# Performance work log

Hardware: AMD Instinct MI355X
Metric: run time of the kernel (lower is better)

The kernel has to match this reference:

```python
import jax, jax.numpy as jnp
import numpy as np
import math

D_MODEL = 1024
NUM_HEADS = 16
D_K = D_MODEL // NUM_HEADS
MAX_SEQ_LEN = 2048
THETA = 10000.0
BATCH = 2
SEQ = 2048


def _rope_tables():
    inv_freq = THETA ** (-jnp.arange(0, D_K, 2, dtype=jnp.float32) / D_K)  # [d_k/2]
    pos = jnp.arange(MAX_SEQ_LEN, dtype=jnp.float32)                      # [max_seq]
    ang = pos[:, None] * inv_freq[None, :]                                # [max_seq, d_k/2]
    return jnp.cos(ang), jnp.sin(ang)


def _apply_rope(x, token_positions, cos_tab, sin_tab):
    # x: [b, h, s, d_k]; token_positions: [b, s]
    cos = cos_tab[token_positions][:, None, :, :]  # [b,1,s,d_k/2]
    sin = sin_tab[token_positions][:, None, :, :]
    xp = x.reshape(*x.shape[:-1], D_K // 2, 2)     # interleaved pairs
    xe, xo = xp[..., 0], xp[..., 1]
    oe = xe * cos - xo * sin
    oo = xe * sin + xo * cos
    return jnp.stack((oe, oo), axis=-1).reshape(x.shape)


def setup_inputs() -> dict:
    key = jax.random.key(0)
    ks = jax.random.split(key, 5)
    std = math.sqrt(2.0 / (D_MODEL + D_MODEL))
    x = jax.random.normal(ks[0], (BATCH, SEQ, D_MODEL), dtype=jnp.float32)
    wq = jax.random.normal(ks[1], (D_MODEL, D_MODEL), dtype=jnp.float32) * std
    wk = jax.random.normal(ks[2], (D_MODEL, D_MODEL), dtype=jnp.float32) * std
    wv = jax.random.normal(ks[3], (D_MODEL, D_MODEL), dtype=jnp.float32) * std
    wo = jax.random.normal(ks[4], (D_MODEL, D_MODEL), dtype=jnp.float32) * std
    token_positions = jnp.broadcast_to(jnp.arange(SEQ, dtype=jnp.int32), (BATCH, SEQ))
    return {"x": x, "wq": wq, "wk": wk, "wv": wv, "wo": wo,
            "token_positions": token_positions}


def reference(x, wq, wk, wv, wo, token_positions):
    b, s, _ = x.shape
    cos_tab, sin_tab = _rope_tables()

    def proj_heads(w):
        y = jnp.einsum('oi,bsi->bso', w, x)  # Linear: w[d_out,d_in]
        return y.reshape(b, s, NUM_HEADS, D_K).transpose(0, 2, 1, 3)  # [b,h,s,d_k]

    q = proj_heads(wq)
    k = proj_heads(wk)
    v = proj_heads(wv)
    q = _apply_rope(q, token_positions, cos_tab, sin_tab)
    k = _apply_rope(k, token_positions, cos_tab, sin_tab)

    scores = jnp.einsum('bhqd,bhkd->bhqk', q, k) / math.sqrt(D_K)
    causal = jnp.tril(jnp.ones((s, s), dtype=bool))
    scores = jnp.where(causal, scores, -jnp.inf)
    attn = jax.nn.softmax(scores, axis=-1)
    out = jnp.einsum('bhqk,bhkd->bhqd', attn, v)
    out = out.transpose(0, 2, 1, 3).reshape(b, s, D_MODEL)
    return jnp.einsum('oi,bsi->bso', wo, out)
```

## Files before the change

kernel.cpp:

```cpp
#include <hip/hip_runtime.h>
#include <cstdint>
#include <cstddef>

#define NH 16
#define DK 64
#define DM 1024
#define SEQL 2048
#define NB 2
#define NR (NB * SEQL)

typedef short bf16x8 __attribute__((ext_vector_type(8)));
typedef float f32x4 __attribute__((ext_vector_type(4)));

static __device__ __forceinline__ float bf2f(short u) {
  union { unsigned int i; float f; } x;
  x.i = ((unsigned int)(unsigned short)u) << 16;
  return x.f;
}
static __device__ __forceinline__ short f2bf(float f) {
  union { unsigned int i; float f; } x;
  x.f = f;
  unsigned int r = x.i + 0x7fffu + ((x.i >> 16) & 1u);
  return (short)(r >> 16);
}
static __device__ __forceinline__ unsigned pk2(float a, float b) {
  return ((unsigned)(unsigned short)f2bf(b) << 16) | (unsigned)(unsigned short)f2bf(a);
}

static __device__ __forceinline__ void store_out(float* p, float v) { *p = v; }
static __device__ __forceinline__ void store_out(short* p, float v) { *p = f2bf(v); }

static __device__ __forceinline__ void gload16(const short* g, short* l) {
  __builtin_amdgcn_global_load_lds((const __attribute__((address_space(1))) void*)g,
                                   (__attribute__((address_space(3))) void*)l, 16, 0, 0);
}

__global__ void cvt_all(const float* __restrict__ x, const float* __restrict__ w0,
                        const float* __restrict__ w1, const float* __restrict__ w2,
                        const float* __restrict__ w3, short* __restrict__ xb,
                        short* __restrict__ o0, short* __restrict__ o1,
                        short* __restrict__ o2, short* __restrict__ o3) {
  int y = blockIdx.y;
  const float* in;
  short* out;
  if (y < 4) { in = x + (size_t)y * DM * DM; out = xb + (size_t)y * DM * DM; }
  else if (y == 4) { in = w0; out = o0; }
  else if (y == 5) { in = w1; out = o1; }
  else if (y == 6) { in = w2; out = o2; }
  else { in = w3; out = o3; }
  int i = (blockIdx.x * blockDim.x + threadIdx.x) * 4;
  float4 v = *reinterpret_cast<const float4*>(in + i);
  short4 o;
  o.x = f2bf(v.x); o.y = f2bf(v.y); o.z = f2bf(v.z); o.w = f2bf(v.w);
  *reinterpret_cast<short4*>(out + i) = o;
}

__global__ void rope_table_kernel(float2* __restrict__ tab) {
  int idx = blockIdx.x * blockDim.x + threadIdx.x;
  int pos = idx >> 5, j = idx & 31;
  float freq = powf(10000.0f, -(float)j / 32.0f);
  float ang = (float)pos * freq;
  tab[idx] = make_float2(cosf(ang), sinf(ang));
}

__global__ void rope_apply_kernel(short* __restrict__ Qb, short* __restrict__ Kb,
                                  const int* __restrict__ pos, const float2* __restrict__ tab) {
  short* buf = blockIdx.y ? Kb : Qb;
  const float scale = blockIdx.y ? 1.0f : 0.1803368801f;
  int gid = blockIdx.x * blockDim.x + threadIdx.x;
  int elem = gid * 8;
  int row = elem >> 10, off = elem & 1023;
  int j0 = (off & 63) >> 1;
  short* ptr = buf + (size_t)row * DM + off;
  bf16x8 v = *reinterpret_cast<bf16x8*>(ptr);
  const float2* tp = &tab[pos[row] * 32 + j0];
  bf16x8 o;
#pragma unroll
  for (int q = 0; q < 4; ++q) {
    float2 cs = tp[q];
    float xe = bf2f(v[2 * q]), xo = bf2f(v[2 * q + 1]);
    o[2 * q] = f2bf((xe * cs.x - xo * cs.y) * scale);
    o[2 * q + 1] = f2bf((xe * cs.y + xo * cs.x) * scale);
  }
  *reinterpret_cast<bf16x8*>(ptr) = o;
}

__global__ __launch_bounds__(256) void vt_transpose_kernel(const short* __restrict__ V,
                                                           short* __restrict__ Vt) {
  __shared__ short tile[64][64];
  const int t = threadIdx.x;
  const int bh = blockIdx.y, b = bh >> 4, h = bh & 15;
  const int st = blockIdx.x * 64;
#pragma unroll
  for (int p = 0; p < 2; ++p) {
    int c = p * 256 + t;
    int srow = c >> 3, ch = c & 7;
    int chs = ch ^ ((srow >> 3) & 7);
    *reinterpret_cast<bf16x8*>(&tile[srow][chs * 8]) =
        *reinterpret_cast<const bf16x8*>(&V[(size_t)(b * SEQL + st + srow) * DM + h * 64 + ch * 8]);
  }
  __syncthreads();
#pragma unroll
  for (int p = 0; p < 2; ++p) {
    int c = p * 256 + t;
    int drow = c >> 3, soff = (c & 7) * 8;
    short o[8];
#pragma unroll
    for (int e = 0; e < 8; ++e) {
      int srow = soff + e;
      int col = (((drow >> 3) ^ ((srow >> 3) & 7)) << 3) + (drow & 7);
      o[e] = tile[srow][col];
    }
    *reinterpret_cast<bf16x8*>(&Vt[(size_t)(bh * DK + drow) * SEQL + st + soff]) =
        *reinterpret_cast<bf16x8*>(o);
  }
}

template <typename OutT>
static __device__ __forceinline__ void gemm_body(const short* __restrict__ A,
                                                 const short* __restrict__ B,
                                                 OutT* __restrict__ C,
                                                 int m0, int n0, int N, int K) {
  __shared__ short As[128][32];
  __shared__ short Bs[128][32];
  const int t = threadIdx.x;
  const int wid = t >> 6, lane = t & 63;
  const int wr = wid >> 1, wc = wid & 1;
  const int lrow = lane & 15, lk = lane >> 4;

  f32x4 acc[4][4];
#pragma unroll
  for (int i = 0; i < 4; ++i)
#pragma unroll
    for (int j = 0; j < 4; ++j) acc[i][j] = (f32x4){0.f, 0.f, 0.f, 0.f};

  for (int k0 = 0; k0 < K; k0 += 32) {
    __syncthreads();
#pragma unroll
    for (int p = 0; p < 2; ++p) {
      int c = p * 256 + t;
      int row = c >> 2, kc = (c & 3) * 8;
      gload16(&A[(size_t)(m0 + row) * K + k0 + kc], &As[0][0] + (size_t)(p * 256 + wid * 64) * 8);
      gload16(&B[(size_t)(n0 + row) * K + k0 + kc], &Bs[0][0] + (size_t)(p * 256 + wid * 64) * 8);
    }
    __syncthreads();
    bf16x8 af[4], bfr[4];
#pragma unroll
    for (int i = 0; i < 4; ++i) {
      af[i] = *reinterpret_cast<const bf16x8*>(&As[wr * 64 + i * 16 + lrow][lk * 8]);
      bfr[i] = *reinterpret_cast<const bf16x8*>(&Bs[wc * 64 + i * 16 + lrow][lk * 8]);
    }
    __builtin_amdgcn_s_setprio(1);
#pragma unroll
    for (int i = 0; i < 4; ++i)
#pragma unroll
      for (int j = 0; j < 4; ++j)
        acc[i][j] = __builtin_amdgcn_mfma_f32_16x16x32_bf16(af[i], bfr[j], acc[i][j], 0, 0, 0);
    __builtin_amdgcn_s_setprio(0);
  }
#pragma unroll
  for (int i = 0; i < 4; ++i)
#pragma unroll
    for (int j = 0; j < 4; ++j) {
      int row = m0 + wr * 64 + i * 16 + lk * 4;
      int col = n0 + wc * 64 + j * 16 + lrow;
#pragma unroll
      for (int r = 0; r < 4; ++r) store_out(&C[(size_t)(row + r) * N + col], acc[i][j][r]);
    }
}

__global__ __launch_bounds__(256) void qkv_gemm_kernel(
    const short* __restrict__ X, const short* __restrict__ Wq, const short* __restrict__ Wk,
    const short* __restrict__ Wv, short* __restrict__ Q, short* __restrict__ K,
    short* __restrict__ V) {
  int nb = blockIdx.x;
  const short* B = (nb < 8) ? Wq : (nb < 16) ? Wk : Wv;
  short* C = (nb < 8) ? Q : (nb < 16) ? K : V;
  gemm_body<short>(X, B, C, blockIdx.y * 128, (nb & 7) * 128, DM, DM);
}

__global__ __launch_bounds__(256) void out_gemm_kernel(const short* __restrict__ A,
                                                       const short* __restrict__ W,
                                                       float* __restrict__ C) {
  gemm_body<float>(A, W, C, blockIdx.y * 128, blockIdx.x * 128, DM, DM);
}

__global__ __launch_bounds__(256) void attn_kernel(const short* __restrict__ Q,
                                                   const short* __restrict__ K,
                                                   const short* __restrict__ Vt,
                                                   short* __restrict__ O) {
  __shared__ short Ks[2][64][72];
  __shared__ short Vs[2][64][72];
  __shared__ short Ps[4][16][72];
  const int t = threadIdx.x;
  const int wid = t >> 6, lane = t & 63;
  const int lrow = lane & 15, lk = lane >> 4;
  const int lin = blockIdx.x + 16 * blockIdx.y;
  const int xcd = lin & 7, idx = lin >> 3;
  const int bh = xcd * 4 + (idx >> 4);
  const int bx = idx & 15;
  const int b = bh >> 4, h = bh & 15;
  const size_t base = (size_t)b * SEQL * DM + (size_t)h * DK;
  const size_t vbase = (size_t)bh * DK * SEQL;
  const int c0 = t, c1 = 256 + t;
  const int kr0 = c0 >> 3, ko0 = (c0 & 7) * 8;
  const int kr1 = c1 >> 3, ko1 = (c1 & 7) * 8;
  const float THR = 11.5416f;

#pragma unroll
  for (int pi = 0; pi < 2; ++pi) {
    const int qt = pi ? (31 - bx) : bx;
    const int qmin = qt * 64 + wid * 16;

    bf16x8 aq[2];
#pragma unroll
    for (int c = 0; c < 2; ++c)
      aq[c] = *reinterpret_cast<const bf16x8*>(
          &Q[base + (size_t)(qmin + lrow) * DM + c * 32 + lk * 8]);

    f32x4 oacc[4];
#pragma unroll
    for (int g = 0; g < 4; ++g) oacc[g] = (f32x4){0.f, 0.f, 0.f, 0.f};
    float mrow = -1e30f, lsum = 0.f;

    __syncthreads();
    {
      bf16x8 k0 = *reinterpret_cast<const bf16x8*>(&K[base + (size_t)kr0 * DM + ko0]);
      bf16x8 k1 = *reinterpret_cast<const bf16x8*>(&K[base + (size_t)kr1 * DM + ko1]);
      bf16x8 v0 = *reinterpret_cast<const bf16x8*>(&Vt[vbase + (size_t)kr0 * SEQL + ko0]);
      bf16x8 v1 = *reinterpret_cast<const bf16x8*>(&Vt[vbase + (size_t)kr1 * SEQL + ko1]);
      *reinterpret_cast<bf16x8*>(&Ks[0][kr0][ko0]) = k0;
      *reinterpret_cast<bf16x8*>(&Ks[0][kr1][ko1]) = k1;
      *reinterpret_cast<bf16x8*>(&Vs[0][kr0][ko0]) = v0;
      *reinterpret_cast<bf16x8*>(&Vs[0][kr1][ko1]) = v1;
    }
    int cur = 0;
    bf16x8 kreg0, kreg1, vreg0, vreg1;
    for (int kt = 0; kt <= qt; ++kt) {
      __syncthreads();
      if (kt < qt) {
        size_t ko = (size_t)(kt + 1) * 64;
        kreg0 = *reinterpret_cast<const bf16x8*>(&K[base + (ko + kr0) * DM + ko0]);
        kreg1 = *reinterpret_cast<const bf16x8*>(&K[base + (ko + kr1) * DM + ko1]);
        vreg0 = *reinterpret_cast<const bf16x8*>(&Vt[vbase + (size_t)kr0 * SEQL + ko + ko0]);
        vreg1 = *reinterpret_cast<const bf16x8*>(&Vt[vbase + (size_t)kr1 * SEQL + ko + ko1]);
      }
      const bool active = (kt * 64 <= qmin + 15);
      if (active) {
        f32x4 st[4];
        __builtin_amdgcn_s_setprio(1);
#pragma unroll
        for (int g = 0; g < 4; ++g) {
          bf16x8 kf0 = *reinterpret_cast<const bf16x8*>(&Ks[cur][g * 16 + lrow][lk * 8]);
          bf16x8 kf1 = *reinterpret_cast<const bf16x8*>(&Ks[cur][g * 16 + lrow][32 + lk * 8]);
          f32x4 z = (f32x4){0.f, 0.f, 0.f, 0.f};
          z = __builtin_amdgcn_mfma_f32_16x16x32_bf16(kf0, aq[0], z, 0, 0, 0);
          st[g] = __builtin_amdgcn_mfma_f32_16x16x32_bf16(kf1, aq[1], z, 0, 0, 0);
        }
        __builtin_amdgcn_s_setprio(0);
        const int qg = qmin + lrow;
        if (kt == qt) {
#pragma unroll
          for (int g = 0; g < 4; ++g)
#pragma unroll
            for (int r = 0; r < 4; ++r)
              if (kt * 64 + g * 16 + lk * 4 + r > qg) st[g][r] = -1e30f;
        }
        float pmax = st[0][0];
#pragma unroll
        for (int g = 0; g < 4; ++g)
#pragma unroll
          for (int r = 0; r < 4; ++r) pmax = fmaxf(pmax, st[g][r]);
        if (!__all(pmax <= mrow + THR)) {
          float mx = pmax;
          mx = fmaxf(mx, __shfl_xor(mx, 16));
          mx = fmaxf(mx, __shfl_xor(mx, 32));
          float mnew = fmaxf(mrow, mx);
          float alpha = exp2f(mrow - mnew);
          lsum *= alpha;
          float alr[4];
#pragma unroll
          for (int r = 0; r < 4; ++r) alr[r] = __shfl(alpha, lk * 4 + r);
#pragma unroll
          for (int g = 0; g < 4; ++g)
#pragma unroll
            for (int r = 0; r < 4; ++r) oacc[g][r] *= alr[r];
          mrow = mnew;
        }
        float p[4][4], psum = 0.f;
#pragma unroll
        for (int g = 0; g < 4; ++g)
#pragma unroll
          for (int r = 0; r < 4; ++r) {
            float e = exp2f(st[g][r] - mrow);
            p[g][r] = e;
            psum += e;
          }
        lsum += psum;
#pragma unroll
        for (int g = 0; g < 4; ++g) {
          uint2 wv = make_uint2(pk2(p[g][0], p[g][1]), pk2(p[g][2], p[g][3]));
          *reinterpret_cast<uint2*>(&Ps[wid][lrow][g * 16 + lk * 4]) = wv;
        }
        asm volatile("s_waitcnt lgkmcnt(0)" ::: "memory");
        __builtin_amdgcn_sched_barrier(0);
        bf16x8 pa0 = *reinterpret_cast<const bf16x8*>(&Ps[wid][lrow][lk * 8]);
        bf16x8 pa1 = *reinterpret_cast<const bf16x8*>(&Ps[wid][lrow][32 + lk * 8]);
        __builtin_amdgcn_s_setprio(1);
#pragma unroll
        for (int g = 0; g < 4; ++g) {
          bf16x8 vf0 = *reinterpret_cast<const bf16x8*>(&Vs[cur][g * 16 + lrow][lk * 8]);
          bf16x8 vf1 = *reinterpret_cast<const bf16x8*>(&Vs[cur][g * 16 + lrow][32 + lk * 8]);
          oacc[g] = __builtin_amdgcn_mfma_f32_16x16x32_bf16(pa0, vf0, oacc[g], 0, 0, 0);
          oacc[g] = __builtin_amdgcn_mfma_f32_16x16x32_bf16(pa1, vf1, oacc[g], 0, 0, 0);
        }
        __builtin_amdgcn_s_setprio(0);
      }
      if (kt < qt) {
        *reinterpret_cast<bf16x8*>(&Ks[cur ^ 1][kr0][ko0]) = kreg0;
        *reinterpret_cast<bf16x8*>(&Ks[cur ^ 1][kr1][ko1]) = kreg1;
        *reinterpret_cast<bf16x8*>(&Vs[cur ^ 1][kr0][ko0]) = vreg0;
        *reinterpret_cast<bf16x8*>(&Vs[cur ^ 1][kr1][ko1]) = vreg1;
      }
      cur ^= 1;
    }
    lsum += __shfl_xor(lsum, 16);
    lsum += __shfl_xor(lsum, 32);
    float lr[4];
#pragma unroll
    for (int r = 0; r < 4; ++r) lr[r] = 1.0f / __shfl(lsum, lk * 4 + r);
#pragma unroll
    for (int g = 0; g < 4; ++g)
#pragma unroll
      for (int r = 0; r < 4; ++r)
        O[base + (size_t)(qmin + lk * 4 + r) * DM + g * 16 + lrow] = f2bf(oacc[g][r] * lr[r]);
  }
}

extern "C" void kernel_launch(void* const* d_in, const int* in_sizes, int n_in,
                              void* d_out, int out_size, void* d_ws, size_t ws_size,
                              hipStream_t stream) {
  const float* x = (const float*)d_in[0];
  const float* wq = (const float*)d_in[1];
  const float* wk = (const float*)d_in[2];
  const float* wv = (const float*)d_in[3];
  const float* wo = (const float*)d_in[4];
  const int* tpos = (const int*)d_in[5];
  float* out = (float*)d_out;

  char* w = (char*)d_ws;
  short* xb = (short*)w;  w += (size_t)NR * DM * 2;
  short* wqb = (short*)w; w += (size_t)DM * DM * 2;
  short* wkb = (short*)w; w += (size_t)DM * DM * 2;
  short* wvb = (short*)w; w += (size_t)DM * DM * 2;
  short* wob = (short*)w; w += (size_t)DM * DM * 2;
  short* Qb = (short*)w;  w += (size_t)NR * DM * 2;
  short* Kb = (short*)w;  w += (size_t)NR * DM * 2;
  short* Vb = (short*)w;  w += (size_t)NR * DM * 2;
  short* Ob = (short*)w;  w += (size_t)NR * DM * 2;
  float2* tab = (float2*)w;
  short* Vtb = xb;

  cvt_all<<<dim3(DM * DM / 1024, 8), 256, 0, stream>>>(x, wq, wk, wv, wo, xb, wqb, wkb, wvb, wob);
  rope_table_kernel<<<2048 * 32 / 256, 256, 0, stream>>>(tab);
  qkv_gemm_kernel<<<dim3(24, NR / 128), 256, 0, stream>>>(xb, wqb, wkb, wvb, Qb, Kb, Vb);
  rope_apply_kernel<<<dim3(NR * DM / 8 / 256, 2), 256, 0, stream>>>(Qb, Kb, tpos, tab);
  vt_transpose_kernel<<<dim3(SEQL / 64, NB * NH), 256, 0, stream>>>(Vb, Vtb);
  attn_kernel<<<dim3(16, 32), 256, 0, stream>>>(Qb, Kb, Vtb, Ob);
  out_gemm_kernel<<<dim3(DM / 128, NR / 128), 256, 0, stream>>>(Ob, wob, out);
}
```

Measured before the change: 136.2 us.

## Split attention into one q-tile per block, longest tiles first, single-buffer LDS

The attention grid changes from 512 blocks that each process a pair of balanced q-tiles to 1024 blocks that each handle one q-tile. Blocks are ordered so the longest causal tiles launch first, spread across XCDs. The K/V LDS tiles drop from double to single buffering with an extra barrier before the refill, which cuts LDS use and may raise occupancy. The per-wave active check is removed, and bf16 packing now uses the v_cvt_pk_bf16_f32 instruction.

```diff
diff --git a/kernel.cpp b/kernel.cpp
--- a/kernel.cpp
+++ b/kernel.cpp
@@ -23,8 +23,10 @@
   unsigned int r = x.i + 0x7fffu + ((x.i >> 16) & 1u);
   return (short)(r >> 16);
 }
-static __device__ __forceinline__ unsigned pk2(float a, float b) {
-  return ((unsigned)(unsigned short)f2bf(b) << 16) | (unsigned)(unsigned short)f2bf(a);
+static __device__ __forceinline__ unsigned cvtpk(float a, float b) {
+  unsigned r;
+  asm("v_cvt_pk_bf16_f32 %0, %1, %2" : "=v"(r) : "v"(a), "v"(b));
+  return r;
 }
 
 static __device__ __forceinline__ void store_out(float* p, float v) { *p = v; }
@@ -189,152 +191,140 @@
                                                    const short* __restrict__ K,
                                                    const short* __restrict__ Vt,
                                                    short* __restrict__ O) {
-  __shared__ short Ks[2][64][72];
-  __shared__ short Vs[2][64][72];
+  __shared__ short Ks[64][72];
+  __shared__ short Vs[64][72];
   __shared__ short Ps[4][16][72];
   const int t = threadIdx.x;
   const int wid = t >> 6, lane = t & 63;
   const int lrow = lane & 15, lk = lane >> 4;
-  const int lin = blockIdx.x + 16 * blockIdx.y;
+  const int lin = blockIdx.x;
   const int xcd = lin & 7, idx = lin >> 3;
-  const int bh = xcd * 4 + (idx >> 4);
-  const int bx = idx & 15;
+  const int qt = 31 - (idx >> 2);
+  const int bh = xcd * 4 + (idx & 3);
   const int b = bh >> 4, h = bh & 15;
   const size_t base = (size_t)b * SEQL * DM + (size_t)h * DK;
   const size_t vbase = (size_t)bh * DK * SEQL;
-  const int c0 = t, c1 = 256 + t;
-  const int kr0 = c0 >> 3, ko0 = (c0 & 7) * 8;
-  const int kr1 = c1 >> 3, ko1 = (c1 & 7) * 8;
+  const int kr0 = t >> 3, kr1 = 32 + (t >> 3), ko0 = (t & 7) * 8;
   const float THR = 11.5416f;
-
-#pragma unroll
-  for (int pi = 0; pi < 2; ++pi) {
-    const int qt = pi ? (31 - bx) : bx;
-    const int qmin = qt * 64 + wid * 16;
-
-    bf16x8 aq[2];
-#pragma unroll
-    for (int c = 0; c < 2; ++c)
-      aq[c] = *reinterpret_cast<const bf16x8*>(
-          &Q[base + (size_t)(qmin + lrow) * DM + c * 32 + lk * 8]);
-
-    f32x4 oacc[4];
-#pragma unroll
-    for (int g = 0; g < 4; ++g) oacc[g] = (f32x4){0.f, 0.f, 0.f, 0.f};
-    float mrow = -1e30f, lsum = 0.f;
-
+  const int qmin = qt * 64 + wid * 16;
+
+  bf16x8 aq[2];
+#pragma unroll
+  for (int c = 0; c < 2; ++c)
+    aq[c] = *reinterpret_cast<const bf16x8*>(
+        &Q[base + (size_t)(qmin + lrow) * DM + c * 32 + lk * 8]);
+
+  f32x4 oacc[4];
+#pragma unroll
+  for (int g = 0; g < 4; ++g) oacc[g] = (f32x4){0.f, 0.f, 0.f, 0.f};
+  float mrow = -1e30f, lsum = 0.f;
+
+  {
+    bf16x8 k0 = *reinterpret_cast<const bf16x8*>(&K[base + (size_t)kr0 * DM + ko0]);
+    bf16x8 k1 = *reinterpret_cast<const bf16x8*>(&K[base + (size_t)kr1 * DM + ko0]);
+    bf16x8 v0 = *reinterpret_cast<const bf16x8*>(&Vt[vbase + (size_t)kr0 * SEQL + ko0]);
+    bf16x8 v1 = *reinterpret_cast<const bf16x8*>(&Vt[vbase + (size_t)kr1 * SEQL + ko0]);
+    *reinterpret_cast<bf16x8*>(&Ks[kr0][ko0]) = k0;
+    *reinterpret_cast<bf16x8*>(&Ks[kr1][ko0]) = k1;
+    *reinterpret_cast<bf16x8*>(&Vs[kr0][ko0]) = v0;
+    *reinterpret_cast<bf16x8*>(&Vs[kr1][ko0]) = v1;
+  }
+  bf16x8 kreg0, kreg1, vreg0, vreg1;
+  for (int kt = 0; kt <= qt; ++kt) {
     __syncthreads();
-    {
-      bf16x8 k0 = *reinterpret_cast<const bf16x8*>(&K[base + (size_t)kr0 * DM + ko0]);
-      bf16x8 k1 = *reinterpret_cast<const bf16x8*>(&K[base + (size_t)kr1 * DM + ko1]);
-      bf16x8 v0 = *reinterpret_cast<const bf16x8*>(&Vt[vbase + (size_t)kr0 * SEQL + ko0]);
-      bf16x8 v1 = *reinterpret_cast<const bf16x8*>(&Vt[vbase + (size_t)kr1 * SEQL + ko1]);
-      *reinterpret_cast<bf16x8*>(&Ks[0][kr0][ko0]) = k0;
-      *reinterpret_cast<bf16x8*>(&Ks[0][kr1][ko1]) = k1;
-      *reinterpret_cast<bf16x8*>(&Vs[0][kr0][ko0]) = v0;
-      *reinterpret_cast<bf16x8*>(&Vs[0][kr1][ko1]) = v1;
-    }
-    int cur = 0;
-    bf16x8 kreg0, kreg1, vreg0, vreg1;
-    for (int kt = 0; kt <= qt; ++kt) {
-      __syncthreads();
-      if (kt < qt) {
-        size_t ko = (size_t)(kt + 1) * 64;
-        kreg0 = *reinterpret_cast<const bf16x8*>(&K[base + (ko + kr0) * DM + ko0]);
-        kreg1 = *reinterpret_cast<const bf16x8*>(&K[base + (ko + kr1) * DM + ko1]);
-        vreg0 = *reinterpret_cast<const bf16x8*>(&Vt[vbase + (size_t)kr0 * SEQL + ko + ko0]);
-        vreg1 = *reinterpret_cast<const bf16x8*>(&Vt[vbase + (size_t)kr1 * SEQL + ko + ko1]);
+    if (kt < qt) {
+      size_t ko = (size_t)(kt + 1) * 64;
+      kreg0 = *reinterpret_cast<const bf16x8*>(&K[base + (ko + kr0) * DM + ko0]);
+      kreg1 = *reinterpret_cast<const bf16x8*>(&K[base + (ko + kr1) * DM + ko0]);
+      vreg0 = *reinterpret_cast<const bf16x8*>(&Vt[vbase + (size_t)kr0 * SEQL + ko + ko0]);
+      vreg1 = *reinterpret_cast<const bf16x8*>(&Vt[vbase + (size_t)kr1 * SEQL + ko + ko0]);
+    }
+    f32x4 st[4];
+    __builtin_amdgcn_s_setprio(1);
+#pragma unroll
+    for (int g = 0; g < 4; ++g) {
+      bf16x8 kf0 = *reinterpret_cast<const bf16x8*>(&Ks[g * 16 + lrow][lk * 8]);
+      bf16x8 kf1 = *reinterpret_cast<const bf16x8*>(&Ks[g * 16 + lrow][32 + lk * 8]);
+      f32x4 z = (f32x4){0.f, 0.f, 0.f, 0.f};
+      z = __builtin_amdgcn_mfma_f32_16x16x32_bf16(kf0, aq[0], z, 0, 0, 0);
+      st[g] = __builtin_amdgcn_mfma_f32_16x16x32_bf16(kf1, aq[1], z, 0, 0, 0);
+    }
+    __builtin_amdgcn_s_setprio(0);
+    const int qg = qmin + lrow;
+    if (kt == qt) {
+#pragma unroll
+      for (int g = 0; g < 4; ++g)
+#pragma unroll
+        for (int r = 0; r < 4; ++r)
+          if (kt * 64 + g * 16 + lk * 4 + r > qg) st[g][r] = -1e30f;
+    }
+    float pmax = st[0][0];
+#pragma unroll
+    for (int g = 0; g < 4; ++g)
+#pragma unroll
+      for (int r = 0; r < 4; ++r) pmax = fmaxf(pmax, st[g][r]);
+    if (!__all(pmax <= mrow + THR)) {
+      float mx = pmax;
+      mx = fmaxf(mx, __shfl_xor(mx, 16));
+      mx = fmaxf(mx, __shfl_xor(mx, 32));
+      float mnew = fmaxf(mrow, mx);
+      float alpha = exp2f(mrow - mnew);
+      lsum *= alpha;
+      float alr[4];
+#pragma unroll
+      for (int r = 0; r < 4; ++r) alr[r] = __shfl(alpha, lk * 4 + r);
+#pragma unroll
+      for (int g = 0; g < 4; ++g)
+#pragma unroll
+        for (int r = 0; r < 4; ++r) oacc[g][r] *= alr[r];
+      mrow = mnew;
+    }
+    float p[4][4], psum = 0.f;
+#pragma unroll
+    for (int g = 0; g < 4; ++g)
+#pragma unroll
+      for (int r = 0; r < 4; ++r) {
+        float e = exp2f(st[g][r] - mrow);
+        p[g][r] = e;
+        psum += e;
       }
-      const bool active = (kt * 64 <= qmin + 15);
-      if (active) {
-        f32x4 st[4];
-        __builtin_amdgcn_s_setprio(1);
-#pragma unroll
-        for (int g = 0; g < 4; ++g) {
-          bf16x8 kf0 = *reinterpret_cast<const bf16x8*>(&Ks[cur][g * 16 + lrow][lk * 8]);
-          bf16x8 kf1 = *reinterpret_cast<const bf16x8*>(&Ks[cur][g * 16 + lrow][32 + lk * 8]);
-          f32x4 z = (f32x4){0.f, 0.f, 0.f, 0.f};
-          z = __builtin_amdgcn_mfma_f32_16x16x32_bf16(kf0, aq[0], z, 0, 0, 0);
-          st[g] = __builtin_amdgcn_mfma_f32_16x16x32_bf16(kf1, aq[1], z, 0, 0, 0);
-        }
-        __builtin_amdgcn_s_setprio(0);
-        const int qg = qmin + lrow;
-        if (kt == qt) {
-#pragma unroll
-          for (int g = 0; g < 4; ++g)
-#pragma unroll
-            for (int r = 0; r < 4; ++r)
-              if (kt * 64 + g * 16 + lk * 4 + r > qg) st[g][r] = -1e30f;
-        }
-        float pmax = st[0][0];
-#pragma unroll
-        for (int g = 0; g < 4; ++g)
-#pragma unroll
-          for (int r = 0; r < 4; ++r) pmax = fmaxf(pmax, st[g][r]);
-        if (!__all(pmax <= mrow + THR)) {
-          float mx = pmax;
-          mx = fmaxf(mx, __shfl_xor(mx, 16));
-          mx = fmaxf(mx, __shfl_xor(mx, 32));
-          float mnew = fmaxf(mrow, mx);
-          float alpha = exp2f(mrow - mnew);
-          lsum *= alpha;
-          float alr[4];
-#pragma unroll
-          for (int r = 0; r < 4; ++r) alr[r] = __shfl(alpha, lk * 4 + r);
-#pragma unroll
-          for (int g = 0; g < 4; ++g)
-#pragma unroll
-            for (int r = 0; r < 4; ++r) oacc[g][r] *= alr[r];
-          mrow = mnew;
-        }
-        float p[4][4], psum = 0.f;
-#pragma unroll
-        for (int g = 0; g < 4; ++g)
-#pragma unroll
-          for (int r = 0; r < 4; ++r) {
-            float e = exp2f(st[g][r] - mrow);
-            p[g][r] = e;
-            psum += e;
-          }
-        lsum += psum;
-#pragma unroll
-        for (int g = 0; g < 4; ++g) {
-          uint2 wv = make_uint2(pk2(p[g][0], p[g][1]), pk2(p[g][2], p[g][3]));
-          *reinterpret_cast<uint2*>(&Ps[wid][lrow][g * 16 + lk * 4]) = wv;
-        }
-        asm volatile("s_waitcnt lgkmcnt(0)" ::: "memory");
-        __builtin_amdgcn_sched_barrier(0);
-        bf16x8 pa0 = *reinterpret_cast<const bf16x8*>(&Ps[wid][lrow][lk * 8]);
-        bf16x8 pa1 = *reinterpret_cast<const bf16x8*>(&Ps[wid][lrow][32 + lk * 8]);
-        __builtin_amdgcn_s_setprio(1);
-#pragma unroll
-        for (int g = 0; g < 4; ++g) {
-          bf16x8 vf0 = *reinterpret_cast<const bf16x8*>(&Vs[cur][g * 16 + lrow][lk * 8]);
-          bf16x8 vf1 = *reinterpret_cast<const bf16x8*>(&Vs[cur][g * 16 + lrow][32 + lk * 8]);
-          oacc[g] = __builtin_amdgcn_mfma_f32_16x16x32_bf16(pa0, vf0, oacc[g], 0, 0, 0);
-          oacc[g] = __builtin_amdgcn_mfma_f32_16x16x32_bf16(pa1, vf1, oacc[g], 0, 0, 0);
-        }
-        __builtin_amdgcn_s_setprio(0);
-      }
-      if (kt < qt) {
-        *reinterpret_cast<bf16x8*>(&Ks[cur ^ 1][kr0][ko0]) = kreg0;
-        *reinterpret_cast<bf16x8*>(&Ks[cur ^ 1][kr1][ko1]) = kreg1;
-        *reinterpret_cast<bf16x8*>(&Vs[cur ^ 1][kr0][ko0]) = vreg0;
-        *reinterpret_cast<bf16x8*>(&Vs[cur ^ 1][kr1][ko1]) = vreg1;
-      }
-      cur ^= 1;
-    }
-    lsum += __shfl_xor(lsum, 16);
-    lsum += __shfl_xor(lsum, 32);
-    float lr[4];
-#pragma unroll
-    for (int r = 0; r < 4; ++r) lr[r] = 1.0f / __shfl(lsum, lk * 4 + r);
-#pragma unroll
-    for (int g = 0; g < 4; ++g)
-#pragma unroll
-      for (int r = 0; r < 4; ++r)
-        O[base + (size_t)(qmin + lk * 4 + r) * DM + g * 16 + lrow] = f2bf(oacc[g][r] * lr[r]);
-  }
+    lsum += psum;
+#pragma unroll
+    for (int g = 0; g < 4; ++g) {
+      uint2 wv = make_uint2(cvtpk(p[g][0], p[g][1]), cvtpk(p[g][2], p[g][3]));
+      *reinterpret_cast<uint2*>(&Ps[wid][lrow][g * 16 + lk * 4]) = wv;
+    }
+    asm volatile("s_waitcnt lgkmcnt(0)" ::: "memory");
+    __builtin_amdgcn_sched_barrier(0);
+    bf16x8 pa0 = *reinterpret_cast<const bf16x8*>(&Ps[wid][lrow][lk * 8]);
+    bf16x8 pa1 = *reinterpret_cast<const bf16x8*>(&Ps[wid][lrow][32 + lk * 8]);
+    __builtin_amdgcn_s_setprio(1);
+#pragma unroll
+    for (int g = 0; g < 4; ++g) {
+      bf16x8 vf0 = *reinterpret_cast<const bf16x8*>(&Vs[g * 16 + lrow][lk * 8]);
+      bf16x8 vf1 = *reinterpret_cast<const bf16x8*>(&Vs[g * 16 + lrow][32 + lk * 8]);
+      oacc[g] = __builtin_amdgcn_mfma_f32_16x16x32_bf16(pa0, vf0, oacc[g], 0, 0, 0);
+      oacc[g] = __builtin_amdgcn_mfma_f32_16x16x32_bf16(pa1, vf1, oacc[g], 0, 0, 0);
+    }
+    __builtin_amdgcn_s_setprio(0);
+    __syncthreads();
+    if (kt < qt) {
+      *reinterpret_cast<bf16x8*>(&Ks[kr0][ko0]) = kreg0;
+      *reinterpret_cast<bf16x8*>(&Ks[kr1][ko0]) = kreg1;
+      *reinterpret_cast<bf16x8*>(&Vs[kr0][ko0]) = vreg0;
+      *reinterpret_cast<bf16x8*>(&Vs[kr1][ko0]) = vreg1;
+    }
+  }
+  lsum += __shfl_xor(lsum, 16);
+  lsum += __shfl_xor(lsum, 32);
+  float lr[4];
+#pragma unroll
+  for (int r = 0; r < 4; ++r) lr[r] = 1.0f / __shfl(lsum, lk * 4 + r);
+#pragma unroll
+  for (int g = 0; g < 4; ++g)
+#pragma unroll
+    for (int r = 0; r < 4; ++r)
+      O[base + (size_t)(qmin + lk * 4 + r) * DM + g * 16 + lrow] = f2bf(oacc[g][r] * lr[r]);
 }
 
 extern "C" void kernel_launch(void* const* d_in, const int* in_sizes, int n_in,
@@ -366,6 +356,6 @@
   qkv_gemm_kernel<<<dim3(24, NR / 128), 256, 0, stream>>>(xb, wqb, wkb, wvb, Qb, Kb, Vb);
   rope_apply_kernel<<<dim3(NR * DM / 8 / 256, 2), 256, 0, stream>>>(Qb, Kb, tpos, tab);
   vt_transpose_kernel<<<dim3(SEQL / 64, NB * NH), 256, 0, stream>>>(Vb, Vtb);
-  attn_kernel<<<dim3(16, 32), 256, 0, stream>>>(Qb, Kb, Vtb, Ob);
+  attn_kernel<<<1024, 256, 0, stream>>>(Qb, Kb, Vtb, Ob);
   out_gemm_kernel<<<dim3(DM / 128, NR / 128), 256, 0, stream>>>(Ob, wob, out);
 }
```

New measurement: 133.9 us. No clear change (-1.7%).
